# Optimization experiments

Hardware: AMD Instinct MI355X
Metric: run time of the kernel (lower is better)

## Reference

```python
import jax, jax.numpy as jnp
import numpy as np

E, N, C, A, S, H, HD, RH = 320000, 20000, 128, 4, 16, 8, 32, 64
AH = H * HD  # 256 attn-head channels; mul_alpha = AH, mul_alpha_head = HD
OUT = 128


def smooth_leaky_relu(x, a=0.2):
    # Equiformer SmoothLeakyReLU: 0.5*((1+a)*x + (1-a)*x*(2*sigmoid(x)-1))
    return 0.5 * ((1 + a) * x + (1 - a) * x * (2.0 * jax.nn.sigmoid(x) - 1.0))


def setup_inputs() -> dict:
    key = jax.random.key(0)
    ks = jax.random.split(key, 20)
    d = {
        'message': jax.random.normal(ks[0], (E, C), jnp.float32),
        'edge_attr': jax.random.normal(ks[1], (E, A), jnp.float32),
        'edge_scalars': jax.random.normal(ks[2], (E, S), jnp.float32),
        'w_rad1': jax.random.normal(ks[3], (S, RH), jnp.float32) / np.sqrt(S),
        'b_rad1': jnp.zeros((RH,), jnp.float32),
        'w_rad2': jax.random.normal(ks[4], (RH, C * A), jnp.float32) / np.sqrt(RH),
        'b_rad2': jnp.zeros((C * A,), jnp.float32),
        'w_dtp_v': jax.random.normal(ks[5], (C, A), jnp.float32) / np.sqrt(A),
        'w_lin_act': jax.random.normal(ks[6], (C, C), jnp.float32) / np.sqrt(C),
        'b_lin_act': jnp.zeros((C,), jnp.float32),
        'w_alpha': jax.random.normal(ks[7], (C, AH), jnp.float32) / np.sqrt(C),
        'b_alpha': jnp.zeros((AH,), jnp.float32),
        'w_lin_v': jax.random.normal(ks[8], (C, AH), jnp.float32) / np.sqrt(C),
        'b_lin_v': jnp.zeros((AH,), jnp.float32),
        'alpha_dot': jax.random.normal(ks[9], (H, HD), jnp.float32) / np.sqrt(HD),
        'w_proj': jax.random.normal(ks[10], (AH, OUT), jnp.float32) / np.sqrt(AH),
        'b_proj': jnp.zeros((OUT,), jnp.float32),
        'edge_dst': jax.random.randint(ks[11], (E,), 0, N, jnp.int32),
        'n_nodes_dst': N,
    }
    return d


def reference(message, edge_attr, edge_scalars,
              w_rad1, b_rad1, w_rad2, b_rad2,
              w_dtp_v, w_lin_act, b_lin_act,
              w_alpha, b_alpha, w_lin_v, b_lin_v,
              alpha_dot, w_proj, b_proj,
              edge_dst, n_nodes_dst):
    n = n_nodes_dst
    # dtp_rad: radial MLP -> per-edge depthwise TP weights [E, C, A]
    h = jax.nn.silu(edge_scalars @ w_rad1 + b_rad1)
    w = (h @ w_rad2 + b_rad2).reshape(-1, C, A)
    # sep_act.dtp (scalar irreps): out[e,c] = msg[e,c] * sum_a w[e,c,a]*attr[e,a]
    msg = message * jnp.einsum('eca,ea->ec', w, edge_attr)
    # sep_alpha -> alpha heads [E, H, HD]
    alpha = (msg @ w_alpha + b_alpha).reshape(-1, H, HD)
    # sep_act.lin + gate (scalars -> SiLU)
    value = jax.nn.silu(msg @ w_lin_act + b_lin_act)
    # sep_value: internal-weight dtp then linear, reshape to heads
    value = value * jnp.einsum('ca,ea->ec', w_dtp_v, edge_attr)
    value = (value @ w_lin_v + b_lin_v).reshape(-1, H, HD)
    # attention logits
    alpha = smooth_leaky_relu(alpha)
    alpha = jnp.einsum('ehk,hk->eh', alpha, alpha_dot)
    # scatter softmax over destination nodes
    amax = jax.ops.segment_max(alpha, edge_dst, num_segments=n)  # [N, H]
    amax = jnp.where(jnp.isfinite(amax), amax, 0.0)
    ex = jnp.exp(alpha - amax[edge_dst])
    denom = jax.ops.segment_sum(ex, edge_dst, num_segments=n)
    alpha = ex / (denom[edge_dst] + 1e-16)
    # weighted scatter-add aggregation
    attn = value * alpha[..., None]  # [E, H, HD]
    node = jax.ops.segment_sum(attn, edge_dst, num_segments=n)  # [N, H, HD]
    node = node.reshape(n, AH)  # heads2vec
    return node @ w_proj + b_proj
```

## Files before the change

kernel.cpp:

```cpp
#include <hip/hip_runtime.h>
#include <hip/hip_bf16.h>

#define C_   128
#define A_   4
#define S_   16
#define RH_  64
#define H_   8
#define AH_  256
#define OUT_ 128

typedef __attribute__((ext_vector_type(8))) short bf16x8;
typedef __attribute__((ext_vector_type(4))) float f32x4;

__device__ __forceinline__ float sigf(float x) { return 1.0f / (1.0f + __expf(-x)); }

__device__ __forceinline__ unsigned short f2bf(float x) {
    unsigned u = __float_as_uint(x);
    unsigned r = (u + 0x7fffu + ((u >> 16) & 1u)) >> 16;
    return (unsigned short)r;
}

__device__ __forceinline__ unsigned pkbf(float a, float b) {
    union { __hip_bfloat162 h; unsigned u; } c;
    c.h = __float22bfloat162_rn(float2{a, b});
    return c.u;
}

__device__ __forceinline__ unsigned enc(float x) {
    unsigned b = __float_as_uint(x);
    return (b & 0x80000000u) ? ~b : (b | 0x80000000u);
}
__device__ __forceinline__ float dec(unsigned u) {
    unsigned b = (u & 0x80000000u) ? (u & 0x7fffffffu) : ~u;
    return __uint_as_float(b);
}

__global__ void k_pack(const float* __restrict__ W, short* __restrict__ out, int K, int N) {
    const int KS = K / 32;
    const int ct = blockIdx.x / KS, ks = blockIdx.x % KS;
    const int l = threadIdx.x, lr = l & 15, lg = l >> 4;
    bf16x8 v;
    #pragma unroll
    for (int j = 0; j < 8; j++)
        v[j] = (short)f2bf(W[(size_t)(ks * 32 + lg * 8 + j) * N + ct * 16 + lr]);
    *(bf16x8*)&out[((size_t)blockIdx.x * 64 + l) * 8] = v;
}

__global__ void k_pack_dtp(const float* __restrict__ W, short* __restrict__ out) {
    const int ct = blockIdx.x >> 3, ks = blockIdx.x & 7;
    const int l = threadIdx.x, lr = l & 15, lg = l >> 4;
    bf16x8 v;
    #pragma unroll
    for (int j = 0; j < 8; j++)
        v[j] = (short)f2bf(W[(size_t)(ks * 8 + lg * 2 + (j >> 2)) * 512 + (ct * 16 + lr) * 4 + (j & 3)]);
    *(bf16x8*)&out[((size_t)blockIdx.x * 64 + l) * 8] = v;
}

__global__ __launch_bounds__(256) void k_hist(
    const int* __restrict__ edge_dst, int* __restrict__ deg, int E)
{
    const int e = blockIdx.x * 256 + threadIdx.x;
    if (e < E) atomicAdd(&deg[edge_dst[e]], 1);
}

__global__ __launch_bounds__(1024) void k_scan(
    const int* __restrict__ deg, int* __restrict__ cursor, int N)
{
    __shared__ int part[1024];
    const int t = threadIdx.x;
    const int per = (N + 1023) / 1024;
    const int i0 = t * per;
    int s = 0;
    for (int i = 0; i < per; i++) { int idx = i0 + i; if (idx < N) s += deg[idx]; }
    part[t] = s;
    __syncthreads();
    for (int off = 1; off < 1024; off <<= 1) {
        int v = (t >= off) ? part[t - off] : 0;
        __syncthreads();
        part[t] += v;
        __syncthreads();
    }
    int excl = (t == 0) ? 0 : part[t - 1];
    for (int i = 0; i < per; i++) {
        int idx = i0 + i;
        if (idx < N) { cursor[idx] = excl; excl += deg[idx]; }
    }
}

__global__ __launch_bounds__(256) void k_fill(
    const int* __restrict__ edge_dst, int* __restrict__ cursor,
    int* __restrict__ sorted, int E)
{
    const int e = blockIdx.x * 256 + threadIdx.x;
    if (e < E) {
        const int pos = atomicAdd(&cursor[edge_dst[e]], 1);
        sorted[pos] = e;
    }
}

__global__ __launch_bounds__(256, 4) void k_msgalpha(
    const float* __restrict__ message, const float* __restrict__ edge_attr,
    const float* __restrict__ edge_scalars,
    const float* __restrict__ w_rad1, const float* __restrict__ b_rad1,
    const short* __restrict__ w_rad2_lin, const float* __restrict__ b_rad2,
    const short* __restrict__ w_alpha_lin, const float* __restrict__ b_alpha,
    const float* __restrict__ alpha_dot, const int* __restrict__ edge_dst,
    short* __restrict__ msg_bf, float* __restrict__ logits, unsigned* __restrict__ amax_u)
{
    __shared__ __align__(16) char smem[25216];
    short* Ap     = (short*)smem;
    short* msg_s  = (short*)(smem + 16384);
    float* w1_s   = (float*)(smem + 16384);
    float* es_s   = (float*)(smem + 16384 + 4096);
    float* attr_s = (float*)(smem + 24576);
    int*   dst_s  = (int*)(smem + 25088);

    const int t = threadIdx.x;
    const long e0 = (long)blockIdx.x * 32;

    *(float4*)&w1_s[t * 4] = *(const float4*)&w_rad1[t * 4];
    if (t < 128) {
        const int r = t >> 2, s4 = (t & 3) * 4;
        *(float4*)&es_s[r * 17 + s4] = *(const float4*)&edge_scalars[(e0 + r) * S_ + s4];
    }
    if (t < 32) {
        *(float4*)&attr_s[t * 4] = *(const float4*)&edge_attr[(e0 + t) * A_];
        dst_s[t] = edge_dst[e0 + t];
    }
    __syncthreads();

    {
        const int r = t & 31, o0 = (t >> 5) * 8;
        float acc[8];
        #pragma unroll
        for (int i = 0; i < 8; i++) acc[i] = b_rad1[o0 + i];
        #pragma unroll
        for (int s = 0; s < S_; s++) {
            const float ev = es_s[r * 17 + s];
            #pragma unroll
            for (int i = 0; i < 8; i++) acc[i] += ev * w1_s[s * 64 + o0 + i];
        }
        float h[8];
        #pragma unroll
        for (int i = 0; i < 8; i++) { const float x = acc[i]; h[i] = x * sigf(x); }
        const float4 a4 = *(const float4*)&attr_s[r * 4];
        char* base = (char*)Ap + r * 512;
        const int sw = (r & 31) << 4;
        #pragma unroll
        for (int c = 0; c < 4; c++) {
            const float h0 = h[2 * c], h1 = h[2 * c + 1];
            uint4 v;
            v.x = pkbf(h0 * a4.x, h0 * a4.y);
            v.y = pkbf(h0 * a4.z, h0 * a4.w);
            v.z = pkbf(h1 * a4.x, h1 * a4.y);
            v.w = pkbf(h1 * a4.z, h1 * a4.w);
            *(uint4*)(base + ((o0 * 8 + c * 16) ^ sw)) = v;
        }
    }
    __syncthreads();

    const int w = t >> 6, l = t & 63, lr = l & 15, lg = l >> 4;

    {
        #pragma unroll
        for (int q = 0; q < 2; q++) {
            const int ct = w * 2 + q;
            bf16x8 bf[8];
            #pragma unroll
            for (int ks = 0; ks < 8; ks++)
                bf[ks] = *(const bf16x8*)&w_rad2_lin[((size_t)(ct * 8 + ks) * 64 + l) * 8];
            const int col = ct * 16 + lr;
            const float4 b2 = *(const float4*)&b_rad2[col * 4];
            #pragma unroll
            for (int rt = 0; rt < 2; rt++) {
                const int arow = rt * 16 + lr;
                const char* abase = (char*)Ap + arow * 512;
                const int asw = (arow & 31) << 4;
                bf16x8 af[8];
                #pragma unroll
                for (int ks = 0; ks < 8; ks++)
                    af[ks] = *(const bf16x8*)(abase + ((ks * 64 + lg * 16) ^ asw));
                f32x4 acc = {0.f, 0.f, 0.f, 0.f};
                #pragma unroll
                for (int ks = 0; ks < 8; ks++)
                    acc = __builtin_amdgcn_mfma_f32_16x16x32_bf16(af[ks], bf[ks], acc, 0, 0, 0);
                #pragma unroll
                for (int r = 0; r < 4; r++) {
                    const int row = rt * 16 + lg * 4 + r;
                    const float4 a4 = *(const float4*)&attr_s[row * 4];
                    const float badj = a4.x * b2.x + a4.y * b2.y + a4.z * b2.z + a4.w * b2.w;
                    const float m = message[(e0 + row) * C_ + col];
                    *(short*)((char*)msg_s + row * 256 + ((col * 2) ^ ((row & 15) << 4))) =
                        (short)f2bf(m * (acc[r] + badj));
                }
            }
        }
    }
    __syncthreads();

    {
        #pragma unroll
        for (int i = 0; i < 2; i++) {
            const int q = t + i * 256;
            const int row = q >> 4, ch = q & 15;
            const uint4 v = *(const uint4*)((char*)msg_s + row * 256 + ((ch * 16) ^ ((row & 15) << 4)));
            *(uint4*)((char*)msg_bf + ((e0 + row) * 256 + ch * 16)) = v;
        }
    }

    {
        #pragma unroll
        for (int hq = 0; hq < 2; hq++) {
            const int hd = w * 2 + hq;
            bf16x8 waf[2][4];
            float4 ba4[2], ad4[2];
            #pragma unroll
            for (int q = 0; q < 2; q++) {
                const int ctw = hd * 2 + q;
                #pragma unroll
                for (int ks = 0; ks < 4; ks++)
                    waf[q][ks] = *(const bf16x8*)&w_alpha_lin[((size_t)(ctw * 4 + ks) * 64 + l) * 8];
                ba4[q] = *(const float4*)&b_alpha[ctw * 16 + lg * 4];
                ad4[q] = *(const float4*)&alpha_dot[ctw * 16 + lg * 4];
            }
            #pragma unroll
            for (int ct = 0; ct < 2; ct++) {
                const int erow = ct * 16 + lr;
                const char* mbase = (char*)msg_s + erow * 256;
                const int msw = (erow & 15) << 4;
                bf16x8 mb[4];
                #pragma unroll
                for (int ks = 0; ks < 4; ks++)
                    mb[ks] = *(const bf16x8*)(mbase + ((ks * 64 + lg * 16) ^ msw));
                float s = 0.f;
                #pragma unroll
                for (int q = 0; q < 2; q++) {
                    f32x4 acc = {0.f, 0.f, 0.f, 0.f};
                    #pragma unroll
                    for (int ks = 0; ks < 4; ks++)
                        acc = __builtin_amdgcn_mfma_f32_16x16x32_bf16(waf[q][ks], mb[ks], acc, 0, 0, 0);
                    #pragma unroll
                    for (int r = 0; r < 4; r++) {
                        const float x = acc[r] + ((const float*)&ba4[q])[r];
                        const float y = x * (0.2f + 0.8f * sigf(x));
                        s += y * ((const float*)&ad4[q])[r];
                    }
                }
                s += __shfl_xor(s, 16);
                s += __shfl_xor(s, 32);
                if (lg == 0) {
                    const long e = e0 + ct * 16 + lr;
                    logits[e * H_ + hd] = s;
                    atomicMax(&amax_u[dst_s[ct * 16 + lr] * H_ + hd], enc(s));
                }
            }
        }
    }
}

__global__ __launch_bounds__(256) void k_denom(
    const float* __restrict__ logits, const int* __restrict__ edge_dst,
    const unsigned* __restrict__ amax_u, float* __restrict__ denom, int EH)
{
    const int t = blockIdx.x * 256 + threadIdx.x;
    if (t >= EH) return;
    const int e = t >> 3, h = t & 7;
    const int n = edge_dst[e];
    const float am = dec(amax_u[n * H_ + h]);
    atomicAdd(&denom[n * H_ + h], __expf(logits[t] - am));
}

__global__ __launch_bounds__(512, 2) void k_value(
    const short* __restrict__ msg_bf, const float* __restrict__ edge_attr,
    const short* __restrict__ w_lin_act_lin, const float* __restrict__ b_lin_act,
    const float* __restrict__ w_dtp_v,
    const short* __restrict__ w_lin_v_lin, const float* __restrict__ b_lin_v,
    const float* __restrict__ logits, const int* __restrict__ edge_dst,
    const unsigned* __restrict__ amax_u, const float* __restrict__ denom,
    const int* __restrict__ sorted, float* __restrict__ node)
{
    __shared__ __align__(16) char pool[66560];
    __shared__ float attr_s[64][4];
    __shared__ float wgt_s[64][H_];
    __shared__ int   dst_s[64];
    __shared__ int   eid_s[64];
    short* a_s  = (short*)pool;
    short* v_s  = (short*)(pool + 16384);
    float* val2 = (float*)pool;

    const int t = threadIdx.x;
    const int b0 = blockIdx.x * 64;

    if (t < 64) {
        const int e = sorted[b0 + t];
        eid_s[t] = e;
        dst_s[t] = edge_dst[e];
        *(float4*)&attr_s[t][0] = *(const float4*)&edge_attr[(long)e * A_];
    }
    __syncthreads();
    #pragma unroll
    for (int i = 0; i < 2; i++) {
        const int q = t + i * 512;
        const int row = q >> 4, ch = q & 15;
        const uint4 v = *(const uint4*)((const char*)msg_bf + ((long)eid_s[row] * 256 + ch * 16));
        *(uint4*)((char*)a_s + row * 256 + ((ch * 16) ^ ((row & 15) << 4))) = v;
    }
    {
        const int el = t >> 3, h = t & 7;
        const long e = eid_s[el];
        const int n = dst_s[el];
        const float am = dec(amax_u[n * H_ + h]);
        const float d  = denom[n * H_ + h];
        wgt_s[el][h] = __expf(logits[e * H_ + h] - am) / (d + 1e-16f);
    }
    __syncthreads();

    const int w = t >> 6, l = t & 63, lr = l & 15, lg = l >> 4;
    {
        bf16x8 bfg[4];
        #pragma unroll
        for (int ks = 0; ks < 4; ks++)
            bfg[ks] = *(const bf16x8*)&w_lin_act_lin[((size_t)(w * 4 + ks) * 64 + l) * 8];
        const int col = w * 16 + lr;
        const float bb = b_lin_act[col];
        const float4 wv = *(const float4*)&w_dtp_v[col * 4];
        #pragma unroll
        for (int rt = 0; rt < 4; rt++) {
            const int arow = rt * 16 + lr;
            bf16x8 af[4];
            #pragma unroll
            for (int ks = 0; ks < 4; ks++)
                af[ks] = *(bf16x8*)((char*)a_s + arow * 256 + ((ks * 64 + lg * 16) ^ ((arow & 15) << 4)));
            f32x4 acc = {0.f, 0.f, 0.f, 0.f};
            #pragma unroll
            for (int ks = 0; ks < 4; ks++)
                acc = __builtin_amdgcn_mfma_f32_16x16x32_bf16(af[ks], bfg[ks], acc, 0, 0, 0);
            #pragma unroll
            for (int r = 0; r < 4; r++) {
                const int row = rt * 16 + lg * 4 + r;
                float x = acc[r] + bb;
                x = x * sigf(x);
                const float4 a4 = *(const float4*)&attr_s[row][0];
                const float dv = wv.x * a4.x + wv.y * a4.y + wv.z * a4.z + wv.w * a4.w;
                *(short*)((char*)v_s + row * 256 + ((col * 2) ^ ((row & 15) << 4))) =
                    (short)f2bf(x * dv);
            }
        }
    }
    __syncthreads();

    bf16x8 vf[4][4];
    #pragma unroll
    for (int rt = 0; rt < 4; rt++)
        #pragma unroll
        for (int ks = 0; ks < 4; ks++) {
            const int row = rt * 16 + lr;
            vf[rt][ks] = *(bf16x8*)((char*)v_s + row * 256 + ((ks * 64 + lg * 16) ^ ((row & 15) << 4)));
        }
    __syncthreads();

    #pragma unroll
    for (int q = 0; q < 2; q++) {
        const int ct = w * 2 + q;
        bf16x8 bf[4];
        #pragma unroll
        for (int ks = 0; ks < 4; ks++)
            bf[ks] = *(const bf16x8*)&w_lin_v_lin[((size_t)(ct * 4 + ks) * 64 + l) * 8];
        const int col = ct * 16 + lr;
        const float bb = b_lin_v[col];
        #pragma unroll
        for (int rt = 0; rt < 4; rt++) {
            f32x4 acc = {0.f, 0.f, 0.f, 0.f};
            #pragma unroll
            for (int ks = 0; ks < 4; ks++)
                acc = __builtin_amdgcn_mfma_f32_16x16x32_bf16(vf[rt][ks], bf[ks], acc, 0, 0, 0);
            #pragma unroll
            for (int r = 0; r < 4; r++) {
                const int row = rt * 16 + lg * 4 + r;
                val2[row * 260 + col] = (acc[r] + bb) * wgt_s[row][col >> 5];
            }
        }
    }
    __syncthreads();
    {
        const int c = t & 255, eS = (t >> 8) * 32, eE = eS + 32;
        float run = 0.f;
        int s = eS;
        #pragma unroll 1
        for (int e = eS; e < eE; e++) {
            run += val2[e * 260 + c];
            const bool end = (e == eE - 1) || (dst_s[e + 1] != dst_s[e]);
            if (end) {
                float* np = node + (long)dst_s[e] * AH_ + c;
                if (s == eS || e == eE - 1) atomicAdd(np, run);
                else *np = run;
                run = 0.f; s = e + 1;
            }
        }
    }
}

__global__ __launch_bounds__(256) void k_proj(
    const float* __restrict__ node, const float* __restrict__ w_proj,
    const float* __restrict__ b_proj, float* __restrict__ out)
{
    __shared__ float node_s[32][AH_];
    const int t = threadIdx.x;
    const long n0 = (long)blockIdx.x * 32;
    #pragma unroll
    for (int i = 0; i < 8; i++) {
        const int idx = t + i * 256;
        const int nl = idx >> 6, c4 = (idx & 63) * 4;
        *(float4*)&node_s[nl][c4] = *(const float4*)&node[(n0 + nl) * AH_ + c4];
    }
    __syncthreads();
    const int j0 = (t & 31) * 4;
    const int g  = t >> 5;
    float4 acc4[4];
    const float4 b = *(const float4*)&b_proj[j0];
    #pragma unroll
    for (int i = 0; i < 4; i++) acc4[i] = b;
    const float* wp = w_proj + j0;
    for (int c4 = 0; c4 < 64; c4++) {
        const float4 w0 = *(const float4*)&wp[(c4 * 4 + 0) * OUT_];
        const float4 w1 = *(const float4*)&wp[(c4 * 4 + 1) * OUT_];
        const float4 w2 = *(const float4*)&wp[(c4 * 4 + 2) * OUT_];
        const float4 w3 = *(const float4*)&wp[(c4 * 4 + 3) * OUT_];
        #pragma unroll
        for (int i = 0; i < 4; i++) {
            const float4 nv = *(const float4*)&node_s[g * 4 + i][c4 * 4];
            acc4[i].x += nv.x * w0.x + nv.y * w1.x + nv.z * w2.x + nv.w * w3.x;
            acc4[i].y += nv.x * w0.y + nv.y * w1.y + nv.z * w2.y + nv.w * w3.y;
            acc4[i].z += nv.x * w0.z + nv.y * w1.z + nv.z * w2.z + nv.w * w3.z;
            acc4[i].w += nv.x * w0.w + nv.y * w1.w + nv.z * w2.w + nv.w * w3.w;
        }
    }
    #pragma unroll
    for (int i = 0; i < 4; i++) {
        const long n = n0 + g * 4 + i;
        *(float4*)&out[n * OUT_ + j0] = acc4[i];
    }
}

extern "C" void kernel_launch(void* const* d_in, const int* in_sizes, int n_in,
                              void* d_out, int out_size, void* d_ws, size_t ws_size,
                              hipStream_t stream)
{
    const float* message      = (const float*)d_in[0];
    const float* edge_attr    = (const float*)d_in[1];
    const float* edge_scalars = (const float*)d_in[2];
    const float* w_rad1       = (const float*)d_in[3];
    const float* b_rad1       = (const float*)d_in[4];
    const float* w_rad2       = (const float*)d_in[5];
    const float* b_rad2       = (const float*)d_in[6];
    const float* w_dtp_v      = (const float*)d_in[7];
    const float* w_lin_act    = (const float*)d_in[8];
    const float* b_lin_act    = (const float*)d_in[9];
    const float* w_alpha      = (const float*)d_in[10];
    const float* b_alpha      = (const float*)d_in[11];
    const float* w_lin_v      = (const float*)d_in[12];
    const float* b_lin_v      = (const float*)d_in[13];
    const float* alpha_dot    = (const float*)d_in[14];
    const float* w_proj       = (const float*)d_in[15];
    const float* b_proj       = (const float*)d_in[16];
    const int*   edge_dst     = (const int*)d_in[17];

    const int E = in_sizes[0] / C_;
    const int N = out_size / OUT_;

    char* ws = (char*)d_ws;
    float*    node     = (float*)ws;
    unsigned* amax_u   = (unsigned*)(node + (size_t)N * AH_);
    float*    denom    = (float*)(amax_u + (size_t)N * H_);
    int*      deg      = (int*)(denom + (size_t)N * H_);
    int*      cursor   = deg + N;
    int*      sorted   = cursor + N;
    short*    w_rad2_l = (short*)(sorted + E);
    short*    w_alph_l = w_rad2_l + 64 * 512;
    short*    w_lact_l = w_alph_l + 128 * 256;
    short*    w_linv_l = w_lact_l + 128 * 128;
    short*    msg_bf   = w_linv_l + 128 * 256;
    float*    logits   = (float*)(msg_bf + (size_t)E * C_);

    hipMemsetAsync(d_ws, 0, (size_t)N * (AH_ + 2 * H_ + 1) * 4, stream);

    const int nbE256 = (E + 255) / 256;
    k_pack_dtp<<<64, 64, 0, stream>>>(w_rad2, w_rad2_l);
    k_pack<<<(256/16)*(128/32), 64, 0, stream>>>(w_alpha,   w_alph_l, 128, 256);
    k_pack<<<(128/16)*(128/32), 64, 0, stream>>>(w_lin_act, w_lact_l, 128, 128);
    k_pack<<<(256/16)*(128/32), 64, 0, stream>>>(w_lin_v,   w_linv_l, 128, 256);
    k_hist<<<nbE256, 256, 0, stream>>>(edge_dst, deg, E);
    k_scan<<<1, 1024, 0, stream>>>(deg, cursor, N);
    k_fill<<<nbE256, 256, 0, stream>>>(edge_dst, cursor, sorted, E);
    k_msgalpha<<<E / 32, 256, 0, stream>>>(message, edge_attr, edge_scalars,
                                           w_rad1, b_rad1, w_rad2_l, b_rad2,
                                           w_alph_l, b_alpha, alpha_dot, edge_dst,
                                           msg_bf, logits, amax_u);
    k_denom<<<(E * H_ + 255) / 256, 256, 0, stream>>>(logits, edge_dst, amax_u, denom, E * H_);
    k_value<<<E / 64, 512, 0, stream>>>(msg_bf, edge_attr, w_lact_l, b_lin_act, w_dtp_v,
                                        w_linv_l, b_lin_v, logits, edge_dst, amax_u, denom,
                                        sorted, node);
    k_proj<<<N / 32, 256, 0, stream>>>(node, w_proj, b_proj, (float*)d_out);
}
```

Baseline: 421.5 us.

## Shrink k_value tiles to 32 edges per block and stage weighted values in bf16

k_value now handles 32 edges per 256-thread block instead of 64 edges per 512 threads, with each wave covering two column tiles over two row tiles. The weighted value staging buffer moves from fp32 to bf16, which cuts shared memory from about 66KB to about 17KB and allows more blocks per CU (launch bounds 256,5). The aim is higher occupancy and less LDS pressure. In exchange, node rows shared across tile boundaries need more atomics, and the summed values lose precision from bf16 rounding.

```diff
diff --git a/kernel.cpp b/kernel.cpp
--- a/kernel.cpp
+++ b/kernel.cpp
@@ -18,6 +18,9 @@
     unsigned u = __float_as_uint(x);
     unsigned r = (u + 0x7fffu + ((u >> 16) & 1u)) >> 16;
     return (unsigned short)r;
+}
+__device__ __forceinline__ float bf2f(unsigned short v) {
+    return __uint_as_float((unsigned)v << 16);
 }
 
 __device__ __forceinline__ unsigned pkbf(float a, float b) {
@@ -270,7 +273,7 @@
     atomicAdd(&denom[n * H_ + h], __expf(logits[t] - am));
 }
 
-__global__ __launch_bounds__(512, 2) void k_value(
+__global__ __launch_bounds__(256, 5) void k_value(
     const short* __restrict__ msg_bf, const float* __restrict__ edge_attr,
     const short* __restrict__ w_lin_act_lin, const float* __restrict__ b_lin_act,
     const float* __restrict__ w_dtp_v,
@@ -279,19 +282,19 @@
     const unsigned* __restrict__ amax_u, const float* __restrict__ denom,
     const int* __restrict__ sorted, float* __restrict__ node)
 {
-    __shared__ __align__(16) char pool[66560];
-    __shared__ float attr_s[64][4];
-    __shared__ float wgt_s[64][H_];
-    __shared__ int   dst_s[64];
-    __shared__ int   eid_s[64];
+    __shared__ __align__(16) char pool[16896];
+    __shared__ float attr_s[32][4];
+    __shared__ float wgt_s[32][H_];
+    __shared__ int   dst_s[32];
+    __shared__ int   eid_s[32];
     short* a_s  = (short*)pool;
-    short* v_s  = (short*)(pool + 16384);
-    float* val2 = (float*)pool;
+    short* v_s  = (short*)(pool + 8192);
+    short* val2 = (short*)pool;
 
     const int t = threadIdx.x;
-    const int b0 = blockIdx.x * 64;
-
-    if (t < 64) {
+    const int b0 = blockIdx.x * 32;
+
+    if (t < 32) {
         const int e = sorted[b0 + t];
         eid_s[t] = e;
         dst_s[t] = edge_dst[e];
@@ -300,7 +303,7 @@
     __syncthreads();
     #pragma unroll
     for (int i = 0; i < 2; i++) {
-        const int q = t + i * 512;
+        const int q = t + i * 256;
         const int row = q >> 4, ch = q & 15;
         const uint4 v = *(const uint4*)((const char*)msg_bf + ((long)eid_s[row] * 256 + ch * 16));
         *(uint4*)((char*)a_s + row * 256 + ((ch * 16) ^ ((row & 15) << 4))) = v;
@@ -317,41 +320,48 @@
 
     const int w = t >> 6, l = t & 63, lr = l & 15, lg = l >> 4;
     {
-        bf16x8 bfg[4];
-        #pragma unroll
-        for (int ks = 0; ks < 4; ks++)
-            bfg[ks] = *(const bf16x8*)&w_lin_act_lin[((size_t)(w * 4 + ks) * 64 + l) * 8];
-        const int col = w * 16 + lr;
-        const float bb = b_lin_act[col];
-        const float4 wv = *(const float4*)&w_dtp_v[col * 4];
-        #pragma unroll
-        for (int rt = 0; rt < 4; rt++) {
-            const int arow = rt * 16 + lr;
-            bf16x8 af[4];
+        bf16x8 af[2][4];
+        #pragma unroll
+        for (int rt = 0; rt < 2; rt++)
+            #pragma unroll
+            for (int ks = 0; ks < 4; ks++) {
+                const int arow = rt * 16 + lr;
+                af[rt][ks] = *(bf16x8*)((char*)a_s + arow * 256 + ((ks * 64 + lg * 16) ^ ((arow & 15) << 4)));
+            }
+        #pragma unroll
+        for (int q = 0; q < 2; q++) {
+            const int ct = w * 2 + q;
+            bf16x8 bfg[4];
             #pragma unroll
             for (int ks = 0; ks < 4; ks++)
-                af[ks] = *(bf16x8*)((char*)a_s + arow * 256 + ((ks * 64 + lg * 16) ^ ((arow & 15) << 4)));
-            f32x4 acc = {0.f, 0.f, 0.f, 0.f};
-            #pragma unroll
-            for (int ks = 0; ks < 4; ks++)
-                acc = __builtin_amdgcn_mfma_f32_16x16x32_bf16(af[ks], bfg[ks], acc, 0, 0, 0);
-            #pragma unroll
-            for (int r = 0; r < 4; r++) {
-                const int row = rt * 16 + lg * 4 + r;
-                float x = acc[r] + bb;
-                x = x * sigf(x);
-                const float4 a4 = *(const float4*)&attr_s[row][0];
-                const float dv = wv.x * a4.x + wv.y * a4.y + wv.z * a4.z + wv.w * a4.w;
-                *(short*)((char*)v_s + row * 256 + ((col * 2) ^ ((row & 15) << 4))) =
-                    (short)f2bf(x * dv);
-            }
-        }
-    }
-    __syncthreads();
-
-    bf16x8 vf[4][4];
-    #pragma unroll
-    for (int rt = 0; rt < 4; rt++)
+                bfg[ks] = *(const bf16x8*)&w_lin_act_lin[((size_t)(ct * 4 + ks) * 64 + l) * 8];
+            const int col = ct * 16 + lr;
+            const float bb = b_lin_act[col];
+            const float4 wv = *(const float4*)&w_dtp_v[col * 4];
+            #pragma unroll
+            for (int rt = 0; rt < 2; rt++) {
+                f32x4 acc = {0.f, 0.f, 0.f, 0.f};
+                #pragma unroll
+                for (int ks = 0; ks < 4; ks++)
+                    acc = __builtin_amdgcn_mfma_f32_16x16x32_bf16(af[rt][ks], bfg[ks], acc, 0, 0, 0);
+                #pragma unroll
+                for (int r = 0; r < 4; r++) {
+                    const int row = rt * 16 + lg * 4 + r;
+                    float x = acc[r] + bb;
+                    x = x * sigf(x);
+                    const float4 a4 = *(const float4*)&attr_s[row][0];
+                    const float dv = wv.x * a4.x + wv.y * a4.y + wv.z * a4.z + wv.w * a4.w;
+                    *(short*)((char*)v_s + row * 256 + ((col * 2) ^ ((row & 15) << 4))) =
+                        (short)f2bf(x * dv);
+                }
+            }
+        }
+    }
+    __syncthreads();
+
+    bf16x8 vf[2][4];
+    #pragma unroll
+    for (int rt = 0; rt < 2; rt++)
         #pragma unroll
         for (int ks = 0; ks < 4; ks++) {
             const int row = rt * 16 + lr;
@@ -360,8 +370,8 @@
     __syncthreads();
 
     #pragma unroll
-    for (int q = 0; q < 2; q++) {
-        const int ct = w * 2 + q;
+    for (int q = 0; q < 4; q++) {
+        const int ct = w * 4 + q;
         bf16x8 bf[4];
         #pragma unroll
         for (int ks = 0; ks < 4; ks++)
@@ -369,7 +379,7 @@
         const int col = ct * 16 + lr;
         const float bb = b_lin_v[col];
         #pragma unroll
-        for (int rt = 0; rt < 4; rt++) {
+        for (int rt = 0; rt < 2; rt++) {
             f32x4 acc = {0.f, 0.f, 0.f, 0.f};
             #pragma unroll
             for (int ks = 0; ks < 4; ks++)
@@ -377,22 +387,22 @@
             #pragma unroll
             for (int r = 0; r < 4; r++) {
                 const int row = rt * 16 + lg * 4 + r;
-                val2[row * 260 + col] = (acc[r] + bb) * wgt_s[row][col >> 5];
-            }
-        }
-    }
-    __syncthreads();
-    {
-        const int c = t & 255, eS = (t >> 8) * 32, eE = eS + 32;
+                val2[row * 264 + col] = (short)f2bf((acc[r] + bb) * wgt_s[row][col >> 5]);
+            }
+        }
+    }
+    __syncthreads();
+    {
+        const int c = t;
         float run = 0.f;
-        int s = eS;
+        int s = 0;
         #pragma unroll 1
-        for (int e = eS; e < eE; e++) {
-            run += val2[e * 260 + c];
-            const bool end = (e == eE - 1) || (dst_s[e + 1] != dst_s[e]);
+        for (int e = 0; e < 32; e++) {
+            run += bf2f((unsigned short)val2[e * 264 + c]);
+            const bool end = (e == 31) || (dst_s[e + 1] != dst_s[e]);
             if (end) {
                 float* np = node + (long)dst_s[e] * AH_ + c;
-                if (s == eS || e == eE - 1) atomicAdd(np, run);
+                if (s == 0 || e == 31) atomicAdd(np, run);
                 else *np = run;
                 run = 0.f; s = e + 1;
             }
@@ -497,7 +507,7 @@
                                            w_alph_l, b_alpha, alpha_dot, edge_dst,
                                            msg_bf, logits, amax_u);
     k_denom<<<(E * H_ + 255) / 256, 256, 0, stream>>>(logits, edge_dst, amax_u, denom, E * H_);
-    k_value<<<E / 64, 512, 0, stream>>>(msg_bf, edge_attr, w_lact_l, b_lin_act, w_dtp_v,
+    k_value<<<E / 32, 256, 0, stream>>>(msg_bf, edge_attr, w_lact_l, b_lin_act, w_dtp_v,
                                         w_linv_l, b_lin_v, logits, edge_dst, amax_u, denom,
                                         sorted, node);
     k_proj<<<N / 32, 256, 0, stream>>>(node, w_proj, b_proj, (float*)d_out);
```

Measured after the change: 407.2 us. 1.04x faster.
